# Kernel tuning notes

Hardware: AMD Instinct MI355X
Metric: run time of the kernel (lower is better)

Reference implementation:

```python
import jax, jax.numpy as jnp
import numpy as np

B, N, L, D, DP, H = 1, 128, 256, 256, 128, 8
DH = D // H
LN_EPS = 1e-5


def setup_inputs() -> dict:
    key = jax.random.key(0)
    ks = jax.random.split(key, 8)
    w = lambda k, shape: jax.random.normal(k, shape, jnp.float32) * 0.02
    return {
        "msa": jax.random.normal(ks[0], (B, N, L, D), jnp.float32),
        "pair_bias": jax.random.normal(ks[1], (B, L, L, DP), jnp.float32),
        "msa_mask": jnp.ones((B, N, L), jnp.int32),
        "ln_g": jnp.ones((D,), jnp.float32),
        "ln_b": jnp.zeros((D,), jnp.float32),
        "Wq": w(ks[2], (D, D)), "bq": jnp.zeros((D,), jnp.float32),
        "Wk": w(ks[3], (D, D)), "bk": jnp.zeros((D,), jnp.float32),
        "Wv": w(ks[4], (D, D)), "bv": jnp.zeros((D,), jnp.float32),
        "Wb": w(ks[5], (DP, H)), "bb": jnp.zeros((H,), jnp.float32),
        "Wo": w(ks[6], (D, D)), "bo": jnp.zeros((D,), jnp.float32),
        # gate initialized as in the torch module: zero weight, ones bias
        "Wg": jnp.zeros((D, D), jnp.float32), "bg": jnp.ones((D,), jnp.float32),
    }


def reference(msa, pair_bias, msa_mask, ln_g, ln_b, Wq, bq, Wk, bk, Wv, bv,
              Wb, bb, Wo, bo, Wg, bg):
    b, n, l, d = msa.shape
    h = bb.shape[0]
    dh = d // h
    # LayerNorm over d_msa
    mu = msa.mean(-1, keepdims=True)
    var = msa.var(-1, keepdims=True)
    xn = (msa - mu) * jax.lax.rsqrt(var + LN_EPS) * ln_g + ln_b
    # projections -> [b, n, l, h, dh]
    q = (xn @ Wq + bq).reshape(b, n, l, h, dh)
    k = (xn @ Wk + bk).reshape(b, n, l, h, dh)
    v = (xn @ Wv + bv).reshape(b, n, l, h, dh)
    scores = jnp.einsum('bnihd,bnjhd->bnhij', q, k) / jnp.sqrt(jnp.float32(dh))
    # pair bias: [b, l, l, h] -> [b, 1, h, l, l], broadcast over N_seq
    bias = (pair_bias @ Wb + bb).transpose(0, 3, 1, 2)[:, None]
    scores = scores + bias
    # mask over key axis
    mask = msa_mask[:, :, None, None, :].astype(bool)
    scores = jnp.where(mask, scores, jnp.float32(-1e9))
    attn = jax.nn.softmax(scores, axis=-1)  # dropout is identity at eval
    out = jnp.einsum('bnhij,bnjhd->bnihd', attn, v).reshape(b, n, l, d)
    out = out @ Wo + bo
    gate = jax.nn.sigmoid(xn @ Wg + bg)
    return out * gate
```

## Files before the change

### kernel.cpp

```cpp
#include <hip/hip_runtime.h>
#include <hip/hip_bf16.h>

typedef __attribute__((ext_vector_type(4))) float f32x4;
typedef __attribute__((ext_vector_type(16))) float f32x16;
typedef __attribute__((ext_vector_type(8))) __bf16 bf16x8;
typedef __attribute__((ext_vector_type(4))) __bf16 bf16x4;
typedef __attribute__((ext_vector_type(2))) __bf16 bf16x2;
typedef __attribute__((ext_vector_type(4))) unsigned u32x4;
typedef __attribute__((ext_vector_type(2))) unsigned u32x2;

#define VTS 264
#define KLS 40
#define L2E 1.4426950408889634f

#define GLOAD_LDS16(g, l) __builtin_amdgcn_global_load_lds( \
    (const __attribute__((address_space(1))) void*)(g),     \
    (__attribute__((address_space(3))) void*)(l), 16, 0, 0)

#if __has_builtin(__builtin_amdgcn_permlane32_swap)
#define SWP(a, b) { u32x2 _r = __builtin_amdgcn_permlane32_swap((a), (b), false, false); \
                    (a) = _r[0]; (b) = _r[1]; }
#else
#define SWP(a, b) { unsigned _sa = __shfl_xor((a), 32), _sb = __shfl_xor((b), 32); \
                    unsigned _na = hi ? _sb : (a); (b) = hi ? (b) : _sa; (a) = _na; }
#endif
#define SUM32(ts, lrun) { (lrun) += (ts) + __shfl_xor((ts), 32); }

__global__ __launch_bounds__(256) void ln_kernel(
    const float* __restrict__ msa, const float* __restrict__ g,
    const float* __restrict__ b, __bf16* __restrict__ xn)
{
  const int row = blockIdx.x * 4 + (threadIdx.x >> 6);
  const int lane = threadIdx.x & 63;
  f32x4 x = *(const f32x4*)(msa + (size_t)row * 256 + lane * 4);
  float s = x[0] + x[1] + x[2] + x[3];
  float s2 = x[0]*x[0] + x[1]*x[1] + x[2]*x[2] + x[3]*x[3];
#pragma unroll
  for (int d = 32; d >= 1; d >>= 1) {
    s  += __shfl_xor(s, d);
    s2 += __shfl_xor(s2, d);
  }
  const float mu  = s * (1.f / 256.f);
  const float inv = rsqrtf(s2 * (1.f / 256.f) - mu * mu + 1e-5f);
  const f32x4 gv = *(const f32x4*)(g + lane * 4);
  const f32x4 bv = *(const f32x4*)(b + lane * 4);
  bf16x4 o;
#pragma unroll
  for (int j = 0; j < 4; ++j) o[j] = (__bf16)((x[j] - mu) * inv * gv[j] + bv[j]);
  *(bf16x4*)(xn + (size_t)row * 256 + lane * 4) = o;
}

__global__ __launch_bounds__(256) void biasg_kernel(
    const float* __restrict__ pair, const float* __restrict__ Wb,
    const float* __restrict__ bb, float* __restrict__ biasP)
{
  __shared__ float wbs[1024];
  const int t = threadIdx.x;
#pragma unroll
  for (int r2 = 0; r2 < 4; ++r2) wbs[t + 256 * r2] = Wb[t + 256 * r2];
  __syncthreads();
  const int rb = blockIdx.x * 32 + (t >> 3);
  const int g8 = t & 7;
  const float* src = pair + (size_t)rb * 128 + g8 * 16;
  f32x4 pv[4];
#pragma unroll
  for (int c = 0; c < 4; ++c) pv[c] = *(const f32x4*)(src + c * 4);
  float acc[8];
#pragma unroll
  for (int hh = 0; hh < 8; ++hh) acc[hh] = 0.f;
#pragma unroll
  for (int c = 0; c < 4; ++c)
#pragma unroll
    for (int e = 0; e < 4; ++e) {
      const int p = g8 * 16 + c * 4 + e;
      const f32x4 w0 = *(const f32x4*)&wbs[p * 8];
      const f32x4 w1 = *(const f32x4*)&wbs[p * 8 + 4];
#pragma unroll
      for (int hh = 0; hh < 4; ++hh) {
        acc[hh]     += pv[c][e] * w0[hh];
        acc[4 + hh] += pv[c][e] * w1[hh];
      }
    }
#pragma unroll
  for (int d = 1; d <= 4; d <<= 1)
#pragma unroll
    for (int hh = 0; hh < 8; ++hh) acc[hh] += __shfl_xor(acc[hh], d);
  const int i = rb >> 8, j = rb & 255;
  const int kt2 = j >> 5, g2 = (j >> 3) & 3, h2 = (j >> 2) & 1, e2 = j & 3;
  biasP[(((((size_t)g8 * 8 + kt2) * 4 + g2) * 2 + h2) * 256 + i) * 4 + e2] =
      (acc[g8] + bb[g8]) * L2E;
}

__global__ __launch_bounds__(256) void prep_kernel(
    const float* __restrict__ Wq, const float* __restrict__ Wk,
    const float* __restrict__ Wv, const float* __restrict__ Wg,
    const float* __restrict__ Wo, __bf16* __restrict__ Wt)
{
  __shared__ float ts[64][68];
  const int bid = blockIdx.x, t = threadIdx.x;
  const int w = bid >> 4, tile = bid & 15;
  const int kt = (tile >> 2) * 64, nt = (tile & 3) * 64;
  const float* W = (w == 0) ? Wq : (w == 1) ? Wk : (w == 2) ? Wv : (w == 3) ? Wg : Wo;
  const int rsub = t >> 4, c4 = (t & 15) * 4;
#pragma unroll
  for (int i = 0; i < 4; ++i) {
    const int kr = i * 16 + rsub;
    const f32x4 v = *(const f32x4*)(W + (size_t)(kt + kr) * 256 + nt + c4);
#pragma unroll
    for (int e = 0; e < 4; ++e) ts[kr][c4 + e] = v[e];
  }
  __syncthreads();
#pragma unroll
  for (int i = 0; i < 4; ++i) {
    const int nr = i * 16 + rsub;
    bf16x4 o;
#pragma unroll
    for (int e = 0; e < 4; ++e) o[e] = (__bf16)ts[c4 + e][nr];
    *(bf16x4*)(Wt + (size_t)w * 65536 + (size_t)(nt + nr) * 256 + kt + c4) = o;
  }
}

__global__ __launch_bounds__(512, 4) void qkvg_gemm(
    const __bf16* __restrict__ xn, const __bf16* __restrict__ Wt,
    const float* __restrict__ bq, const float* __restrict__ bk,
    const float* __restrict__ bv, const float* __restrict__ bg,
    __bf16* __restrict__ qb, __bf16* __restrict__ kb,
    __bf16* __restrict__ vb, __bf16* __restrict__ gateb)
{
  __shared__ alignas(16) __bf16 Al[256 * 64];
  __shared__ alignas(16) __bf16 Bl[128 * 64];
  const int t = threadIdx.x;
  const int wave = t >> 6, lane = t & 63;
  const int l15 = lane & 15, l16 = lane >> 4;
  const int bid = blockIdx.x;
  const int xcd = bid & 7, idx = bid >> 3;
  const int m0 = (xcd * 16 + (idx & 15)) * 256;
  const int bn = idx >> 4;
  const int w = bn >> 1;
  const int nloc0 = (bn & 1) * 128;
  const __bf16* Wtw = Wt + (size_t)w * 65536;
  const int wm = (wave >> 1) * 64, wn = (wave & 1) * 64;

  const int srow = (lane >> 3);
  const int chunk = ((lane & 7) ^ srow) * 8;

  f32x4 acc[4][4];
#pragma unroll
  for (int i = 0; i < 4; ++i)
#pragma unroll
    for (int j = 0; j < 4; ++j) acc[i][j] = (f32x4){0.f, 0.f, 0.f, 0.f};

  for (int kt = 0; kt < 4; ++kt) {
    const int k0 = kt * 64;
#pragma unroll
    for (int i = 0; i < 4; ++i) {
      const int row = (wave * 4 + i) * 8 + srow;
      GLOAD_LDS16(xn + (size_t)(m0 + row) * 256 + k0 + chunk, &Al[(wave * 4 + i) * 512]);
    }
#pragma unroll
    for (int i = 0; i < 2; ++i) {
      const int row = (wave * 2 + i) * 8 + srow;
      GLOAD_LDS16(Wtw + (size_t)(nloc0 + row) * 256 + k0 + chunk, &Bl[(wave * 2 + i) * 512]);
    }
    __syncthreads();
#pragma unroll
    for (int kk = 0; kk < 2; ++kk) {
      bf16x8 a[4], bfr[4];
#pragma unroll
      for (int mi = 0; mi < 4; ++mi) {
        const int row = wm + mi * 16 + l15;
        a[mi] = *(const bf16x8*)&Al[row * 64 + ((kk * 32 + l16 * 8) ^ ((row & 7) << 3))];
      }
#pragma unroll
      for (int ni = 0; ni < 4; ++ni) {
        const int row = wn + ni * 16 + l15;
        bfr[ni] = *(const bf16x8*)&Bl[row * 64 + ((kk * 32 + l16 * 8) ^ ((row & 7) << 3))];
      }
#pragma unroll
      for (int mi = 0; mi < 4; ++mi)
#pragma unroll
        for (int ni = 0; ni < 4; ++ni)
          acc[mi][ni] = __builtin_amdgcn_mfma_f32_16x16x32_bf16(a[mi], bfr[ni], acc[mi][ni], 0, 0, 0);
    }
    __syncthreads();
  }

  const float* bias_arr = (w == 0) ? bq : (w == 1) ? bk : (w == 2) ? bv : bg;
  float bnis[4];
#pragma unroll
  for (int ni = 0; ni < 4; ++ni) bnis[ni] = bias_arr[nloc0 + wn + ni * 16 + l15];
  const float qscale = 0.17677669529663687f * L2E;

#pragma unroll
  for (int mi = 0; mi < 4; ++mi)
#pragma unroll
    for (int ni = 0; ni < 4; ++ni)
#pragma unroll
      for (int r = 0; r < 4; ++r) {
        const int grow = m0 + wm + mi * 16 + l16 * 4 + r;
        const int gcol = nloc0 + wn + ni * 16 + l15;
        const float v = acc[mi][ni][r] + bnis[ni];
        const int n = grow >> 8, i2 = grow & 255, h = gcol >> 5, dh = gcol & 31;
        const size_t hoff = (((size_t)n * 8 + h) * 256 + i2) * 32 + dh;
        if (w == 0)      qb[hoff] = (__bf16)(v * qscale);
        else if (w == 1) kb[hoff] = (__bf16)v;
        else if (w == 2) vb[hoff] = (__bf16)v;
        else gateb[(size_t)grow * 256 + gcol] = (__bf16)(1.f / (1.f + __expf(-v)));
      }
}

__device__ __forceinline__ unsigned pk2(float a, float b) {
  bf16x2 t; t[0] = (__bf16)a; t[1] = (__bf16)b;
  return __builtin_bit_cast(unsigned, t);
}

__global__ __launch_bounds__(512, 4) void attn_kernel(
    const __bf16* __restrict__ qb, const __bf16* __restrict__ kb,
    const __bf16* __restrict__ vb, const float* __restrict__ biasP,
    const int* __restrict__ mask, __bf16* __restrict__ opre)
{
  __shared__ alignas(16) __bf16 Kl[256 * KLS];
  __shared__ alignas(16) __bf16 Vt[32 * VTS];
  __shared__ alignas(16) float Ml[256];
  const int t = threadIdx.x, wave = t >> 6, lane = t & 63;
  const int l31 = lane & 31, hi = lane >> 5;
  const int nh = blockIdx.x;
  const int n = nh >> 3, h = nh & 7;
  const __bf16* qbh = qb + (size_t)nh * 8192;

  if (t < 256) {
    const bf16x8* ks = (const bf16x8*)(kb + (size_t)nh * 8192 + t * 32);
    bf16x8 kr[4];
#pragma unroll
    for (int j = 0; j < 4; ++j) kr[j] = ks[j];
#pragma unroll
    for (int j = 0; j < 4; ++j) *(bf16x8*)&Kl[t * KLS + j * 8] = kr[j];
    const bf16x8* vs = (const bf16x8*)(vb + (size_t)nh * 8192 + t * 32);
    bf16x8 vv[4];
#pragma unroll
    for (int j = 0; j < 4; ++j) vv[j] = vs[j];
#pragma unroll
    for (int j = 0; j < 4; ++j)
#pragma unroll
      for (int e = 0; e < 8; ++e) Vt[(j * 8 + e) * VTS + t] = vv[j][e];
    Ml[t] = mask[n * 256 + t] ? 0.f : -1e9f;
  }
  __syncthreads();

  const int q0 = wave * 32;
  const int q = q0 + l31;
  const bf16x8 Qf0 = *(const bf16x8*)(qbh + (size_t)q * 32 + hi * 8);
  const bf16x8 Qf1 = *(const bf16x8*)(qbh + (size_t)q * 32 + 16 + hi * 8);

  const float* bph = biasP + (size_t)h * 65536;

  f32x4 bc[4];
#pragma unroll
  for (int g = 0; g < 4; ++g) {
    const f32x4 bv = *(const f32x4*)(bph + ((g * 2 + hi) * 256 + q) * 4);
    const f32x4 mk = *(const f32x4*)&Ml[8 * g + 4 * hi];
    bc[g] = bv + mk;
  }

  f32x16 Ot;
#pragma unroll
  for (int r = 0; r < 16; ++r) Ot[r] = 0.f;
  float lrun = 0.f;

#pragma unroll 1
  for (int kt = 0; kt < 8; ++kt) {
    const int k0 = kt * 32;
    const int ktn = (kt + 1) & 7;
    const bf16x8 Kf0 = *(const bf16x8*)&Kl[(k0 + l31) * KLS + hi * 8];
    const bf16x8 Kf1 = *(const bf16x8*)&Kl[(k0 + l31) * KLS + 16 + hi * 8];
    const bf16x8 Vf0 = *(const bf16x8*)&Vt[l31 * VTS + k0 + hi * 8];
    const bf16x8 Vf1 = *(const bf16x8*)&Vt[l31 * VTS + k0 + 16 + hi * 8];
    f32x16 st;
#pragma unroll
    for (int g = 0; g < 4; ++g)
#pragma unroll
      for (int e = 0; e < 4; ++e) st[4 * g + e] = bc[g][e];
    st = __builtin_amdgcn_mfma_f32_32x32x16_bf16(Kf0, Qf0, st, 0, 0, 0);
    st = __builtin_amdgcn_mfma_f32_32x32x16_bf16(Kf1, Qf1, st, 0, 0, 0);
#pragma unroll
    for (int g = 0; g < 4; ++g) {
      const f32x4 bv = *(const f32x4*)(bph + (((ktn * 4 + g) * 2 + hi) * 256 + q) * 4);
      const f32x4 mk = *(const f32x4*)&Ml[ktn * 32 + 8 * g + 4 * hi];
      bc[g] = bv + mk;
    }
#pragma unroll
    for (int r = 0; r < 16; ++r) st[r] = exp2f(st[r]);
    float ts = st[0];
#pragma unroll
    for (int r = 1; r < 16; ++r) ts += st[r];
    SUM32(ts, lrun);
    unsigned c0 = pk2(st[0],  st[1]),  c1 = pk2(st[2],  st[3]);
    unsigned c2 = pk2(st[4],  st[5]),  c3 = pk2(st[6],  st[7]);
    unsigned c4 = pk2(st[8],  st[9]),  c5 = pk2(st[10], st[11]);
    unsigned c6 = pk2(st[12], st[13]), c7 = pk2(st[14], st[15]);
    SWP(c0, c2); SWP(c1, c3); SWP(c4, c6); SWP(c5, c7);
    u32x4 w0 = {c0, c1, c2, c3}, w1 = {c4, c5, c6, c7};
    const bf16x8 pf0 = __builtin_bit_cast(bf16x8, w0);
    const bf16x8 pf1 = __builtin_bit_cast(bf16x8, w1);
    Ot = __builtin_amdgcn_mfma_f32_32x32x16_bf16(Vf0, pf0, Ot, 0, 0, 0);
    Ot = __builtin_amdgcn_mfma_f32_32x32x16_bf16(Vf1, pf1, Ot, 0, 0, 0);
  }

  const float invl = 1.f / lrun;
  unsigned P00 = pk2(Ot[0]  * invl, Ot[1]  * invl), P01 = pk2(Ot[2]  * invl, Ot[3]  * invl);
  unsigned P10 = pk2(Ot[4]  * invl, Ot[5]  * invl), P11 = pk2(Ot[6]  * invl, Ot[7]  * invl);
  unsigned P20 = pk2(Ot[8]  * invl, Ot[9]  * invl), P21 = pk2(Ot[10] * invl, Ot[11] * invl);
  unsigned P30 = pk2(Ot[12] * invl, Ot[13] * invl), P31 = pk2(Ot[14] * invl, Ot[15] * invl);
  SWP(P00, P20); SWP(P01, P21); SWP(P10, P30); SWP(P11, P31);
  u32x4 s0 = {P00, P01, P20, P21}, s1 = {P10, P11, P30, P31};
  __bf16* dst = opre + (((size_t)h * 128 + n) * 256 + q) * 32 + hi * 16;
  *(u32x4*)dst = s0;
  *(u32x4*)(dst + 8) = s1;
}

__global__ __launch_bounds__(256) void wo_gemm(
    const __bf16* __restrict__ A, const __bf16* __restrict__ Wtw,
    const float* __restrict__ bo, const __bf16* __restrict__ gateb,
    float* __restrict__ out)
{
  __shared__ alignas(16) __bf16 Al[128 * 64];
  __shared__ alignas(16) __bf16 Bl[128 * 64];
  const int t = threadIdx.x;
  const int wave = t >> 6, lane = t & 63;
  const int l15 = lane & 15, l16 = lane >> 4;
  const int bid = blockIdx.x;
  const int xcd = bid & 7, idx = bid >> 3;
  const int m0 = (xcd * 32 + (idx & 31)) * 128;
  const int nloc0 = (idx >> 5) * 128;
  const int wm = (wave >> 1) * 64, wn = (wave & 1) * 64;

  const int srow = (lane >> 3);
  const int chunk = ((lane & 7) ^ srow) * 8;

  f32x4 acc[4][4];
#pragma unroll
  for (int i = 0; i < 4; ++i)
#pragma unroll
    for (int j = 0; j < 4; ++j) acc[i][j] = (f32x4){0.f, 0.f, 0.f, 0.f};

  for (int kt = 0; kt < 4; ++kt) {
    const int k0 = kt * 64;
#pragma unroll
    for (int i = 0; i < 4; ++i) {
      const int row = wave * 32 + i * 8 + srow;
      const int m = m0 + row;
      const int kg = k0 + chunk;
      GLOAD_LDS16(A + (size_t)(kg >> 5) * 1048576 + (size_t)(m >> 8) * 8192
                    + (m & 255) * 32 + (kg & 31),
                  &Al[(wave * 4 + i) * 512]);
      GLOAD_LDS16(Wtw + (size_t)(nloc0 + row) * 256 + kg, &Bl[(wave * 4 + i) * 512]);
    }
    __syncthreads();
#pragma unroll
    for (int kk = 0; kk < 2; ++kk) {
      bf16x8 a[4], bfr[4];
#pragma unroll
      for (int mi = 0; mi < 4; ++mi) {
        const int row = wm + mi * 16 + l15;
        a[mi] = *(const bf16x8*)&Al[row * 64 + ((kk * 32 + l16 * 8) ^ ((row & 7) << 3))];
      }
#pragma unroll
      for (int ni = 0; ni < 4; ++ni) {
        const int row = wn + ni * 16 + l15;
        bfr[ni] = *(const bf16x8*)&Bl[row * 64 + ((kk * 32 + l16 * 8) ^ ((row & 7) << 3))];
      }
#pragma unroll
      for (int mi = 0; mi < 4; ++mi)
#pragma unroll
        for (int ni = 0; ni < 4; ++ni)
          acc[mi][ni] = __builtin_amdgcn_mfma_f32_16x16x32_bf16(a[mi], bfr[ni], acc[mi][ni], 0, 0, 0);
    }
    __syncthreads();
  }

  float bov[4];
#pragma unroll
  for (int ni = 0; ni < 4; ++ni) bov[ni] = bo[nloc0 + wn + ni * 16 + l15];
#pragma unroll
  for (int mi = 0; mi < 4; ++mi)
#pragma unroll
    for (int ni = 0; ni < 4; ++ni)
#pragma unroll
      for (int r = 0; r < 4; ++r) {
        const int grow = m0 + wm + mi * 16 + l16 * 4 + r;
        const int gcol = nloc0 + wn + ni * 16 + l15;
        const size_t o = (size_t)grow * 256 + gcol;
        out[o] = (acc[mi][ni][r] + bov[ni]) * (float)gateb[o];
      }
}

extern "C" void kernel_launch(void* const* d_in, const int* in_sizes, int n_in,
                              void* d_out, int out_size, void* d_ws, size_t ws_size,
                              hipStream_t stream)
{
  const float* msa  = (const float*)d_in[0];
  const float* pair = (const float*)d_in[1];
  const int*   mask = (const int*)d_in[2];
  const float* ln_g = (const float*)d_in[3];
  const float* ln_b = (const float*)d_in[4];
  const float* Wq = (const float*)d_in[5];  const float* bq = (const float*)d_in[6];
  const float* Wk = (const float*)d_in[7];  const float* bk = (const float*)d_in[8];
  const float* Wv = (const float*)d_in[9];  const float* bv = (const float*)d_in[10];
  const float* Wb = (const float*)d_in[11]; const float* bb = (const float*)d_in[12];
  const float* Wo = (const float*)d_in[13]; const float* bo = (const float*)d_in[14];
  const float* Wg = (const float*)d_in[15]; const float* bg = (const float*)d_in[16];
  float* out = (float*)d_out;

  char* ws = (char*)d_ws;
  __bf16* xn    = (__bf16*)(ws);
  __bf16* qb    = (__bf16*)(ws + 16777216);
  __bf16* kb    = (__bf16*)(ws + 2 * 16777216);
  __bf16* vb    = (__bf16*)(ws + 3 * 16777216);
  __bf16* opre  = (__bf16*)(ws + 4 * 16777216);
  __bf16* Wt    = (__bf16*)(ws + 5 * 16777216);
  __bf16* gateb = (__bf16*)(ws + 5 * 16777216 + 655360);
  float*  biasP = (float*)(ws + 5 * 16777216 + 655360 + 16777216);

  hipLaunchKernelGGL(ln_kernel,    dim3(8192), dim3(256), 0, stream, msa, ln_g, ln_b, xn);
  hipLaunchKernelGGL(biasg_kernel, dim3(2048), dim3(256), 0, stream, pair, Wb, bb, biasP);
  hipLaunchKernelGGL(prep_kernel,  dim3(80),   dim3(256), 0, stream, Wq, Wk, Wv, Wg, Wo, Wt);
  hipLaunchKernelGGL(qkvg_gemm,   dim3(1024), dim3(512), 0, stream, xn, Wt, bq, bk, bv, bg, qb, kb, vb, gateb);
  hipLaunchKernelGGL(attn_kernel, dim3(1024), dim3(512), 0, stream, qb, kb, vb, biasP, mask, opre);
  hipLaunchKernelGGL(wo_gemm,     dim3(512),  dim3(256), 0, stream, opre, Wt + 4 * 65536, bo, gateb, out);
}
```

Measured before the change: 115.8 us.

## Merge setup kernels and compute the gate GEMM inside the output projection

After: 114.6 us. No clear change (-1.0%).

```diff
diff --git a/kernel.cpp b/kernel.cpp
--- a/kernel.cpp
+++ b/kernel.cpp
@@ -26,106 +26,106 @@
 #endif
 #define SUM32(ts, lrun) { (lrun) += (ts) + __shfl_xor((ts), 32); }
 
-__global__ __launch_bounds__(256) void ln_kernel(
+__global__ __launch_bounds__(256) void setup_kernel(
     const float* __restrict__ msa, const float* __restrict__ g,
-    const float* __restrict__ b, __bf16* __restrict__ xn)
-{
-  const int row = blockIdx.x * 4 + (threadIdx.x >> 6);
-  const int lane = threadIdx.x & 63;
-  f32x4 x = *(const f32x4*)(msa + (size_t)row * 256 + lane * 4);
-  float s = x[0] + x[1] + x[2] + x[3];
-  float s2 = x[0]*x[0] + x[1]*x[1] + x[2]*x[2] + x[3]*x[3];
-#pragma unroll
-  for (int d = 32; d >= 1; d >>= 1) {
-    s  += __shfl_xor(s, d);
-    s2 += __shfl_xor(s2, d);
-  }
-  const float mu  = s * (1.f / 256.f);
-  const float inv = rsqrtf(s2 * (1.f / 256.f) - mu * mu + 1e-5f);
-  const f32x4 gv = *(const f32x4*)(g + lane * 4);
-  const f32x4 bv = *(const f32x4*)(b + lane * 4);
-  bf16x4 o;
-#pragma unroll
-  for (int j = 0; j < 4; ++j) o[j] = (__bf16)((x[j] - mu) * inv * gv[j] + bv[j]);
-  *(bf16x4*)(xn + (size_t)row * 256 + lane * 4) = o;
-}
-
-__global__ __launch_bounds__(256) void biasg_kernel(
+    const float* __restrict__ b, __bf16* __restrict__ xn,
     const float* __restrict__ pair, const float* __restrict__ Wb,
-    const float* __restrict__ bb, float* __restrict__ biasP)
-{
-  __shared__ float wbs[1024];
-  const int t = threadIdx.x;
-#pragma unroll
-  for (int r2 = 0; r2 < 4; ++r2) wbs[t + 256 * r2] = Wb[t + 256 * r2];
-  __syncthreads();
-  const int rb = blockIdx.x * 32 + (t >> 3);
-  const int g8 = t & 7;
-  const float* src = pair + (size_t)rb * 128 + g8 * 16;
-  f32x4 pv[4];
-#pragma unroll
-  for (int c = 0; c < 4; ++c) pv[c] = *(const f32x4*)(src + c * 4);
-  float acc[8];
-#pragma unroll
-  for (int hh = 0; hh < 8; ++hh) acc[hh] = 0.f;
-#pragma unroll
-  for (int c = 0; c < 4; ++c)
-#pragma unroll
-    for (int e = 0; e < 4; ++e) {
-      const int p = g8 * 16 + c * 4 + e;
-      const f32x4 w0 = *(const f32x4*)&wbs[p * 8];
-      const f32x4 w1 = *(const f32x4*)&wbs[p * 8 + 4];
-#pragma unroll
-      for (int hh = 0; hh < 4; ++hh) {
-        acc[hh]     += pv[c][e] * w0[hh];
-        acc[4 + hh] += pv[c][e] * w1[hh];
-      }
-    }
-#pragma unroll
-  for (int d = 1; d <= 4; d <<= 1)
-#pragma unroll
-    for (int hh = 0; hh < 8; ++hh) acc[hh] += __shfl_xor(acc[hh], d);
-  const int i = rb >> 8, j = rb & 255;
-  const int kt2 = j >> 5, g2 = (j >> 3) & 3, h2 = (j >> 2) & 1, e2 = j & 3;
-  biasP[(((((size_t)g8 * 8 + kt2) * 4 + g2) * 2 + h2) * 256 + i) * 4 + e2] =
-      (acc[g8] + bb[g8]) * L2E;
-}
-
-__global__ __launch_bounds__(256) void prep_kernel(
+    const float* __restrict__ bb, float* __restrict__ biasP,
     const float* __restrict__ Wq, const float* __restrict__ Wk,
     const float* __restrict__ Wv, const float* __restrict__ Wg,
     const float* __restrict__ Wo, __bf16* __restrict__ Wt)
 {
-  __shared__ float ts[64][68];
-  const int bid = blockIdx.x, t = threadIdx.x;
-  const int w = bid >> 4, tile = bid & 15;
-  const int kt = (tile >> 2) * 64, nt = (tile & 3) * 64;
-  const float* W = (w == 0) ? Wq : (w == 1) ? Wk : (w == 2) ? Wv : (w == 3) ? Wg : Wo;
-  const int rsub = t >> 4, c4 = (t & 15) * 4;
-#pragma unroll
-  for (int i = 0; i < 4; ++i) {
-    const int kr = i * 16 + rsub;
-    const f32x4 v = *(const f32x4*)(W + (size_t)(kt + kr) * 256 + nt + c4);
-#pragma unroll
-    for (int e = 0; e < 4; ++e) ts[kr][c4 + e] = v[e];
-  }
-  __syncthreads();
-#pragma unroll
-  for (int i = 0; i < 4; ++i) {
-    const int nr = i * 16 + rsub;
-    bf16x4 o;
-#pragma unroll
-    for (int e = 0; e < 4; ++e) o[e] = (__bf16)ts[c4 + e][nr];
-    *(bf16x4*)(Wt + (size_t)w * 65536 + (size_t)(nt + nr) * 256 + kt + c4) = o;
+  __shared__ float smem[64 * 68];
+  const int bid = blockIdx.x;
+  const int t = threadIdx.x;
+  if (bid < 2048) {
+    const int lane = t & 63;
+    const f32x4 gv = *(const f32x4*)(g + lane * 4);
+    const f32x4 bv = *(const f32x4*)(b + lane * 4);
+#pragma unroll
+    for (int it = 0; it < 4; ++it) {
+      const int row = bid * 16 + it * 4 + (t >> 6);
+      f32x4 x = *(const f32x4*)(msa + (size_t)row * 256 + lane * 4);
+      float s = x[0] + x[1] + x[2] + x[3];
+      float s2 = x[0]*x[0] + x[1]*x[1] + x[2]*x[2] + x[3]*x[3];
+#pragma unroll
+      for (int d = 32; d >= 1; d >>= 1) {
+        s  += __shfl_xor(s, d);
+        s2 += __shfl_xor(s2, d);
+      }
+      const float mu  = s * (1.f / 256.f);
+      const float inv = rsqrtf(s2 * (1.f / 256.f) - mu * mu + 1e-5f);
+      bf16x4 o;
+#pragma unroll
+      for (int j = 0; j < 4; ++j) o[j] = (__bf16)((x[j] - mu) * inv * gv[j] + bv[j]);
+      *(bf16x4*)(xn + (size_t)row * 256 + lane * 4) = o;
+    }
+  } else if (bid < 4096) {
+    float* wbs = smem;
+#pragma unroll
+    for (int r2 = 0; r2 < 4; ++r2) wbs[t + 256 * r2] = Wb[t + 256 * r2];
+    __syncthreads();
+    const int rb = (bid - 2048) * 32 + (t >> 3);
+    const int g8 = t & 7;
+    const float* src = pair + (size_t)rb * 128 + g8 * 16;
+    f32x4 pv[4];
+#pragma unroll
+    for (int c = 0; c < 4; ++c) pv[c] = *(const f32x4*)(src + c * 4);
+    float acc[8];
+#pragma unroll
+    for (int hh = 0; hh < 8; ++hh) acc[hh] = 0.f;
+#pragma unroll
+    for (int c = 0; c < 4; ++c)
+#pragma unroll
+      for (int e = 0; e < 4; ++e) {
+        const int p = g8 * 16 + c * 4 + e;
+        const f32x4 w0 = *(const f32x4*)&wbs[p * 8];
+        const f32x4 w1 = *(const f32x4*)&wbs[p * 8 + 4];
+#pragma unroll
+        for (int hh = 0; hh < 4; ++hh) {
+          acc[hh]     += pv[c][e] * w0[hh];
+          acc[4 + hh] += pv[c][e] * w1[hh];
+        }
+      }
+#pragma unroll
+    for (int d = 1; d <= 4; d <<= 1)
+#pragma unroll
+      for (int hh = 0; hh < 8; ++hh) acc[hh] += __shfl_xor(acc[hh], d);
+    const int i = rb >> 8, j = rb & 255;
+    const int kt2 = j >> 5, g2 = (j >> 3) & 3, h2 = (j >> 2) & 1, e2 = j & 3;
+    biasP[(((((size_t)g8 * 8 + kt2) * 4 + g2) * 2 + h2) * 256 + i) * 4 + e2] =
+        (acc[g8] + bb[g8]) * L2E;
+  } else {
+    float (*ts)[68] = (float(*)[68])smem;
+    const int idx = bid - 4096;
+    const int w = idx >> 4, tile = idx & 15;
+    const int kt = (tile >> 2) * 64, nt = (tile & 3) * 64;
+    const float* W = (w == 0) ? Wq : (w == 1) ? Wk : (w == 2) ? Wv : (w == 3) ? Wg : Wo;
+    const int rsub = t >> 4, c4 = (t & 15) * 4;
+#pragma unroll
+    for (int i = 0; i < 4; ++i) {
+      const int kr = i * 16 + rsub;
+      const f32x4 v = *(const f32x4*)(W + (size_t)(kt + kr) * 256 + nt + c4);
+#pragma unroll
+      for (int e = 0; e < 4; ++e) ts[kr][c4 + e] = v[e];
+    }
+    __syncthreads();
+#pragma unroll
+    for (int i = 0; i < 4; ++i) {
+      const int nr = i * 16 + rsub;
+      bf16x4 o;
+#pragma unroll
+      for (int e = 0; e < 4; ++e) o[e] = (__bf16)ts[c4 + e][nr];
+      *(bf16x4*)(Wt + (size_t)w * 65536 + (size_t)(nt + nr) * 256 + kt + c4) = o;
+    }
   }
 }
 
 __global__ __launch_bounds__(512, 4) void qkvg_gemm(
     const __bf16* __restrict__ xn, const __bf16* __restrict__ Wt,
     const float* __restrict__ bq, const float* __restrict__ bk,
-    const float* __restrict__ bv, const float* __restrict__ bg,
-    __bf16* __restrict__ qb, __bf16* __restrict__ kb,
-    __bf16* __restrict__ vb, __bf16* __restrict__ gateb)
+    const float* __restrict__ bv,
+    __bf16* __restrict__ qb, __bf16* __restrict__ kb, __bf16* __restrict__ vb)
 {
   __shared__ alignas(16) __bf16 Al[256 * 64];
   __shared__ alignas(16) __bf16 Bl[128 * 64];
@@ -185,11 +185,12 @@
     __syncthreads();
   }
 
-  const float* bias_arr = (w == 0) ? bq : (w == 1) ? bk : (w == 2) ? bv : bg;
+  const float* bias_arr = (w == 0) ? bq : (w == 1) ? bk : bv;
   float bnis[4];
 #pragma unroll
   for (int ni = 0; ni < 4; ++ni) bnis[ni] = bias_arr[nloc0 + wn + ni * 16 + l15];
   const float qscale = 0.17677669529663687f * L2E;
+  __bf16* db2 = (w == 0) ? qb : (w == 1) ? kb : vb;
 
 #pragma unroll
   for (int mi = 0; mi < 4; ++mi)
@@ -199,13 +200,10 @@
       for (int r = 0; r < 4; ++r) {
         const int grow = m0 + wm + mi * 16 + l16 * 4 + r;
         const int gcol = nloc0 + wn + ni * 16 + l15;
-        const float v = acc[mi][ni][r] + bnis[ni];
+        float v = acc[mi][ni][r] + bnis[ni];
+        if (w == 0) v *= qscale;
         const int n = grow >> 8, i2 = grow & 255, h = gcol >> 5, dh = gcol & 31;
-        const size_t hoff = (((size_t)n * 8 + h) * 256 + i2) * 32 + dh;
-        if (w == 0)      qb[hoff] = (__bf16)(v * qscale);
-        else if (w == 1) kb[hoff] = (__bf16)v;
-        else if (w == 2) vb[hoff] = (__bf16)v;
-        else gateb[(size_t)grow * 256 + gcol] = (__bf16)(1.f / (1.f + __expf(-v)));
+        db2[(((size_t)n * 8 + h) * 256 + i2) * 32 + dh] = (__bf16)v;
       }
 }
 
@@ -290,10 +288,10 @@
     }
 #pragma unroll
     for (int r = 0; r < 16; ++r) st[r] = exp2f(st[r]);
-    float ts = st[0];
-#pragma unroll
-    for (int r = 1; r < 16; ++r) ts += st[r];
-    SUM32(ts, lrun);
+    float ts2 = st[0];
+#pragma unroll
+    for (int r = 1; r < 16; ++r) ts2 += st[r];
+    SUM32(ts2, lrun);
     unsigned c0 = pk2(st[0],  st[1]),  c1 = pk2(st[2],  st[3]);
     unsigned c2 = pk2(st[4],  st[5]),  c3 = pk2(st[6],  st[7]);
     unsigned c4 = pk2(st[8],  st[9]),  c5 = pk2(st[10], st[11]);
@@ -319,12 +317,15 @@
 }
 
 __global__ __launch_bounds__(256) void wo_gemm(
-    const __bf16* __restrict__ A, const __bf16* __restrict__ Wtw,
-    const float* __restrict__ bo, const __bf16* __restrict__ gateb,
+    const __bf16* __restrict__ A, const __bf16* __restrict__ Wto,
+    const __bf16* __restrict__ xn, const __bf16* __restrict__ Wtg,
+    const float* __restrict__ bo, const float* __restrict__ bg,
     float* __restrict__ out)
 {
   __shared__ alignas(16) __bf16 Al[128 * 64];
   __shared__ alignas(16) __bf16 Bl[128 * 64];
+  __shared__ alignas(16) __bf16 Xl[128 * 64];
+  __shared__ alignas(16) __bf16 Gl[128 * 64];
   const int t = threadIdx.x;
   const int wave = t >> 6, lane = t & 63;
   const int l15 = lane & 15, l16 = lane >> 4;
@@ -337,11 +338,14 @@
   const int srow = (lane >> 3);
   const int chunk = ((lane & 7) ^ srow) * 8;
 
-  f32x4 acc[4][4];
+  f32x4 acc[4][4], acg[4][4];
 #pragma unroll
   for (int i = 0; i < 4; ++i)
 #pragma unroll
-    for (int j = 0; j < 4; ++j) acc[i][j] = (f32x4){0.f, 0.f, 0.f, 0.f};
+    for (int j = 0; j < 4; ++j) {
+      acc[i][j] = (f32x4){0.f, 0.f, 0.f, 0.f};
+      acg[i][j] = (f32x4){0.f, 0.f, 0.f, 0.f};
+    }
 
   for (int kt = 0; kt < 4; ++kt) {
     const int k0 = kt * 64;
@@ -353,7 +357,9 @@
       GLOAD_LDS16(A + (size_t)(kg >> 5) * 1048576 + (size_t)(m >> 8) * 8192
                     + (m & 255) * 32 + (kg & 31),
                   &Al[(wave * 4 + i) * 512]);
-      GLOAD_LDS16(Wtw + (size_t)(nloc0 + row) * 256 + kg, &Bl[(wave * 4 + i) * 512]);
+      GLOAD_LDS16(Wto + (size_t)(nloc0 + row) * 256 + kg, &Bl[(wave * 4 + i) * 512]);
+      GLOAD_LDS16(xn + (size_t)m * 256 + kg, &Xl[(wave * 4 + i) * 512]);
+      GLOAD_LDS16(Wtg + (size_t)(nloc0 + row) * 256 + kg, &Gl[(wave * 4 + i) * 512]);
     }
     __syncthreads();
 #pragma unroll
@@ -374,13 +380,31 @@
 #pragma unroll
         for (int ni = 0; ni < 4; ++ni)
           acc[mi][ni] = __builtin_amdgcn_mfma_f32_16x16x32_bf16(a[mi], bfr[ni], acc[mi][ni], 0, 0, 0);
-    }
-    __syncthreads();
-  }
-
-  float bov[4];
-#pragma unroll
-  for (int ni = 0; ni < 4; ++ni) bov[ni] = bo[nloc0 + wn + ni * 16 + l15];
+#pragma unroll
+      for (int mi = 0; mi < 4; ++mi) {
+        const int row = wm + mi * 16 + l15;
+        a[mi] = *(const bf16x8*)&Xl[row * 64 + ((kk * 32 + l16 * 8) ^ ((row & 7) << 3))];
+      }
+#pragma unroll
+      for (int ni = 0; ni < 4; ++ni) {
+        const int row = wn + ni * 16 + l15;
+        bfr[ni] = *(const bf16x8*)&Gl[row * 64 + ((kk * 32 + l16 * 8) ^ ((row & 7) << 3))];
+      }
+#pragma unroll
+      for (int mi = 0; mi < 4; ++mi)
+#pragma unroll
+        for (int ni = 0; ni < 4; ++ni)
+          acg[mi][ni] = __builtin_amdgcn_mfma_f32_16x16x32_bf16(a[mi], bfr[ni], acg[mi][ni], 0, 0, 0);
+    }
+    __syncthreads();
+  }
+
+  float bov[4], bgv[4];
+#pragma unroll
+  for (int ni = 0; ni < 4; ++ni) {
+    bov[ni] = bo[nloc0 + wn + ni * 16 + l15];
+    bgv[ni] = bg[nloc0 + wn + ni * 16 + l15];
+  }
 #pragma unroll
   for (int mi = 0; mi < 4; ++mi)
 #pragma unroll
@@ -390,7 +414,8 @@
         const int grow = m0 + wm + mi * 16 + l16 * 4 + r;
         const int gcol = nloc0 + wn + ni * 16 + l15;
         const size_t o = (size_t)grow * 256 + gcol;
-        out[o] = (acc[mi][ni][r] + bov[ni]) * (float)gateb[o];
+        const float gate = 1.f / (1.f + __expf(-(acg[mi][ni][r] + bgv[ni])));
+        out[o] = (acc[mi][ni][r] + bov[ni]) * gate;
       }
 }
 
@@ -418,13 +443,12 @@
   __bf16* vb    = (__bf16*)(ws + 3 * 16777216);
   __bf16* opre  = (__bf16*)(ws + 4 * 16777216);
   __bf16* Wt    = (__bf16*)(ws + 5 * 16777216);
-  __bf16* gateb = (__bf16*)(ws + 5 * 16777216 + 655360);
-  float*  biasP = (float*)(ws + 5 * 16777216 + 655360 + 16777216);
-
-  hipLaunchKernelGGL(ln_kernel,    dim3(8192), dim3(256), 0, stream, msa, ln_g, ln_b, xn);
-  hipLaunchKernelGGL(biasg_kernel, dim3(2048), dim3(256), 0, stream, pair, Wb, bb, biasP);
-  hipLaunchKernelGGL(prep_kernel,  dim3(80),   dim3(256), 0, stream, Wq, Wk, Wv, Wg, Wo, Wt);
-  hipLaunchKernelGGL(qkvg_gemm,   dim3(1024), dim3(512), 0, stream, xn, Wt, bq, bk, bv, bg, qb, kb, vb, gateb);
+  float*  biasP = (float*)(ws + 5 * 16777216 + 655360);
+
+  hipLaunchKernelGGL(setup_kernel, dim3(4176), dim3(256), 0, stream,
+                     msa, ln_g, ln_b, xn, pair, Wb, bb, biasP, Wq, Wk, Wv, Wg, Wo, Wt);
+  hipLaunchKernelGGL(qkvg_gemm,   dim3(768),  dim3(512), 0, stream, xn, Wt, bq, bk, bv, qb, kb, vb);
   hipLaunchKernelGGL(attn_kernel, dim3(1024), dim3(512), 0, stream, qb, kb, vb, biasP, mask, opre);
-  hipLaunchKernelGGL(wo_gemm,     dim3(512),  dim3(256), 0, stream, opre, Wt + 4 * 65536, bo, gateb, out);
-}
+  hipLaunchKernelGGL(wo_gemm,     dim3(512),  dim3(256), 0, stream,
+                     opre, Wt + 4 * 65536, xn, Wt + 3 * 65536, bo, bg, out);
+}
```
